# Kernel optimization log

Measured on AMD Instinct MI355X. Metric: run time of the kernel, lower is better.

## Reference

```python
import jax, jax.numpy as jnp
import numpy as np

NV, NSEG, SEGSZ, GRID = 778, 16, 49, 32
SCALE_FACTOR = 0.1


def grid_sample_3d(vol, pts):
    """Trilinear grid_sample, align_corners=True, zeros padding.
    vol: [D,H,W]; pts: [N,3] with (x,y,z) in [-1,1] (x indexes W, z indexes D).
    """
    D, H, W = vol.shape
    fx = (pts[:, 0] + 1.0) * 0.5 * (W - 1)
    fy = (pts[:, 1] + 1.0) * 0.5 * (H - 1)
    fz = (pts[:, 2] + 1.0) * 0.5 * (D - 1)
    x0f, y0f, z0f = jnp.floor(fx), jnp.floor(fy), jnp.floor(fz)
    wx, wy, wz = fx - x0f, fy - y0f, fz - z0f
    x0 = x0f.astype(jnp.int32)
    y0 = y0f.astype(jnp.int32)
    z0 = z0f.astype(jnp.int32)
    out = jnp.zeros(pts.shape[0], vol.dtype)
    for dz in (0, 1):
        zz = z0 + dz
        ww_z = wz if dz else (1.0 - wz)
        for dy in (0, 1):
            yy = y0 + dy
            ww_zy = ww_z * (wy if dy else (1.0 - wy))
            for dx in (0, 1):
                xx = x0 + dx
                w = ww_zy * (wx if dx else (1.0 - wx))
                valid = (xx >= 0) & (xx < W) & (yy >= 0) & (yy < H) & (zz >= 0) & (zz < D)
                v = vol[jnp.clip(zz, 0, D - 1), jnp.clip(yy, 0, H - 1), jnp.clip(xx, 0, W - 1)]
                out = out + jnp.where(valid, v, 0.0) * w
    return out


def _boxes(segv):
    # segv: [B,16,S,3] -> center [B,16,3], scale [B,16]  (no_grad in original)
    mn = segv.min(axis=2)
    mx = segv.max(axis=2)
    center = 0.5 * (mn + mx)                       # mean of (min, max)
    scale = (1.0 + SCALE_FACTOR) * 0.5 * (mx - mn).max(axis=-1)
    return jax.lax.stop_gradient(center), jax.lax.stop_gradient(scale)


def _cross_sample(seg_src, center, scale, phi, seg):
    # seg_src [B,I,S,3]; center [B,J,3]; scale [B,J]; phi [J,B,G,G,G]
    B = seg_src.shape[0]
    coords = (seg_src[:, :, None, :, :] - center[:, None, :, None, :]) / scale[:, None, :, None, None]
    pts = coords.transpose(2, 0, 1, 3, 4).reshape(NSEG, B, NSEG * SEGSZ, 3)  # [J,B,M,3]
    vals = jax.vmap(jax.vmap(grid_sample_3d))(phi, pts)                      # [J,B,M]
    vals = vals.reshape(NSEG, B, NSEG, SEGSZ).transpose(1, 2, 0, 3)          # [B,I,J,S]
    phisum = vals.sum(axis=2)                                                # [B,I,S]
    orisum = (vals * scale[:, None, :, None]).sum(axis=2)                    # [B,I,S]
    flat = seg.reshape(-1)
    out = jnp.zeros((B, NV), jnp.float32).at[:, flat].add(phisum.reshape(B, -1))
    ori = jnp.zeros((B, NV), jnp.float32).at[:, flat].add(orisum.reshape(B, -1))
    return out, ori


def setup_inputs() -> dict:
    key = jax.random.key(0)
    k1, k2, k3, k4 = jax.random.split(key, 4)
    bs = 128
    vertices = jax.random.normal(k1, (bs, 2, NV, 3), dtype=jnp.float32)
    seg = jax.random.randint(k2, (NSEG, SEGSZ), 0, NV).astype(jnp.int32)
    phi_right = jax.random.uniform(k3, (NSEG, bs, GRID, GRID, GRID), dtype=jnp.float32)
    phi_left = jax.random.uniform(k4, (NSEG, bs, GRID, GRID, GRID), dtype=jnp.float32)
    return {"vertices": vertices, "phi_right": phi_right, "phi_left": phi_left, "seg": seg}


def reference(vertices, phi_right, phi_left, seg):
    left_vert = vertices[:, 1]   # [B,778,3]
    right_vert = vertices[:, 0]
    segL = left_vert[:, seg]     # [B,16,S,3]
    segR = right_vert[:, seg]
    cL, sL = _boxes(segL)
    cR, sR = _boxes(segR)
    out_left, _ = _cross_sample(segL, cR, sR, phi_right, seg)
    out_right, _ = _cross_sample(segR, cL, sL, phi_left, seg)
    num_hand = 2
    loss = (out_left / num_hand ** 2 + out_right / num_hand ** 2).sum(axis=1)  # [B]
    return loss
```

## Files before the change

kernel.cpp:

```cpp
#include <hip/hip_runtime.h>

#define NVV   778
#define NSEG  16
#define SEGSZ 49
#define GRIDN 32
#define BATCH 128
#define NPTS  (NSEG * SEGSZ)
#define VOLSZ (GRIDN * GRIDN * GRIDN)
#define NBLK  256
#define VPB   16

#define HF (16 * 1024)

typedef __attribute__((address_space(1))) const void* as1_t;
typedef __attribute__((address_space(3))) void* as3_t;

#define STREAM(DST, SRC) \
    { _Pragma("unroll") \
      for (int c_ = 0; c_ < 4; ++c_) { \
        int ch_ = c_ * 16 + wv; \
        __builtin_amdgcn_global_load_lds( \
            (as1_t)((SRC) + ch_ * 256 + lane * 4), \
            (as3_t)((DST) + ch_ * 256), 16, 0, 0); \
      } }

__device__ __forceinline__ float tapxy(const float* slab, int x0, int y0,
                                       float wx, float wy)
{
    float s = 0.f;
    #pragma unroll
    for (int dy = 0; dy < 2; ++dy) {
        int yy = y0 + dy;
        if (yy < 0 || yy >= GRIDN) continue;
        float wyv = dy ? wy : 1.f - wy;
        const float* row = slab + yy * GRIDN;
        #pragma unroll
        for (int dx = 0; dx < 2; ++dx) {
            int xx = x0 + dx;
            if (xx < 0 || xx >= GRIDN) continue;
            s += wyv * (dx ? wx : 1.f - wx) * row[xx];
        }
    }
    return s;
}

__global__ __launch_bounds__(1024, 4) void sample_kernel(
    const float* __restrict__ vertices, const int* __restrict__ seg,
    const float* __restrict__ phiR, const float* __restrict__ phiL,
    float* __restrict__ loss)
{
    __shared__ __align__(16) float R0[HF];
    __shared__ __align__(16) float R1[HF];
    __shared__ float4 sbox[VPB];
    __shared__ float wsum[16];

    const int tid  = threadIdx.x;
    const int bx   = blockIdx.x;
    const int k    = bx & (NSEG - 1);
    const int wv   = tid >> 6;
    const int lane = tid & 63;

    auto phiPtr = [&](int it) {
        int vid  = bx + NBLK * it;
        int b    = (vid >> 4) & (BATCH - 1);
        int pass = vid >> 11;
        return (pass == 0 ? phiR : phiL) + ((size_t)k * BATCH + b) * VOLSZ;
    };

    int pvi = (tid < NPTS) ? seg[tid] : 0;

    int vidw    = bx + NBLK * wv;
    int bbw     = (vidw >> 4) & (BATCH - 1);
    int boxSide = ((vidw >> 11) == 0) ? 0 : 1;
    bool bact   = lane < SEGSZ;
    int bvi     = bact ? seg[k * SEGSZ + lane] : 0;
    const float* bvp = vertices + (((size_t)bbw * 2 + boxSide) * NVV + bvi) * 3;
    float bxx = bvp[0], bxy = bvp[1], bxz = bvp[2];

    float pvx = 0.f, pvy = 0.f, pvz = 0.f;
    if (tid < NPTS) {
        int b0 = (bx >> 4) & (BATCH - 1);
        const float* v = vertices + (((size_t)b0 * 2 + 1) * NVV + pvi) * 3;
        pvx = v[0]; pvy = v[1]; pvz = v[2];
    }

    STREAM(R0, phiPtr(0))

    {
        float mnx = bact ? bxx : 1e30f, mxx = bact ? bxx : -1e30f;
        float mny = bact ? bxy : 1e30f, mxy = bact ? bxy : -1e30f;
        float mnz = bact ? bxz : 1e30f, mxz = bact ? bxz : -1e30f;
        #pragma unroll
        for (int m = 32; m; m >>= 1) {
            mnx = fminf(mnx, __shfl_xor(mnx, m));
            mxx = fmaxf(mxx, __shfl_xor(mxx, m));
            mny = fminf(mny, __shfl_xor(mny, m));
            mxy = fmaxf(mxy, __shfl_xor(mxy, m));
            mnz = fminf(mnz, __shfl_xor(mnz, m));
            mxz = fmaxf(mxz, __shfl_xor(mxz, m));
        }
        if (lane == 0) {
            float ext = fmaxf(fmaxf(mxx - mnx, mxy - mny), mxz - mnz);
            sbox[wv] = make_float4(0.5f * (mnx + mxx), 0.5f * (mny + mxy),
                                   0.5f * (mnz + mxz), 1.0f / (0.55f * ext));
        }
    }

    __syncthreads();

    float nvx = 0.f, nvy = 0.f, nvz = 0.f;

    for (int v = 0; v < VPB; ++v) {
        const bool more = (v + 1 < VPB);

        if (v > 0 && tid == 0) {
            float tot = 0.f;
            #pragma unroll
            for (int i = 0; i < 16; ++i) tot += wsum[i];
            int vidp = bx + NBLK * (v - 1);
            atomicAdd(loss + ((vidp >> 4) & (BATCH - 1)), tot * 0.25f);
        }

        float fx = 0.f, fy = 0.f, fz = -2.f;
        if (tid < NPTS) {
            float4 b4 = sbox[v];
            fx = ((pvx - b4.x) * b4.w + 1.f) * 15.5f;
            fy = ((pvy - b4.y) * b4.w + 1.f) * 15.5f;
            fz = ((pvz - b4.z) * b4.w + 1.f) * 15.5f;
        }
        bool active = (fx > -1.f && fx < 32.f && fy > -1.f && fy < 32.f &&
                       fz > -1.f && fz < 32.f);
        float x0f = floorf(fx), y0f = floorf(fy), z0f = floorf(fz);
        float wx = fx - x0f, wy = fy - y0f, wz = fz - z0f;
        int x0 = (int)x0f, y0 = (int)y0f, z0 = (int)z0f;

        STREAM(R1, phiPtr(v) + HF)

        float acc = 0.f;
        if (active && z0 <= 15) {
            if (z0 >= 0)
                acc += (1.f - wz) * tapxy(R0 + z0 * 1024, x0, y0, wx, wy);
            if (z0 <= 14)
                acc += wz * tapxy(R0 + (z0 + 1) * 1024, x0, y0, wx, wy);
        }

        __syncthreads();

        if (more && tid < NPTS) {
            int vid  = bx + NBLK * (v + 1);
            int b_   = (vid >> 4) & (BATCH - 1);
            int srcS = (vid >> 11) == 0 ? 1 : 0;
            const float* vp = vertices + (((size_t)b_ * 2 + srcS) * NVV + pvi) * 3;
            nvx = vp[0]; nvy = vp[1]; nvz = vp[2];
        }
        if (more) { STREAM(R0, phiPtr(v + 1)) }

        if (active && z0 >= 15) {
            if (z0 >= 16)
                acc += (1.f - wz) * tapxy(R1 + (z0 - 16) * 1024, x0, y0, wx, wy);
            if (z0 <= 30)
                acc += wz * tapxy(R1 + (z0 - 15) * 1024, x0, y0, wx, wy);
        }

        #pragma unroll
        for (int off = 32; off; off >>= 1)
            acc += __shfl_down(acc, off);
        if (lane == 0) wsum[wv] = acc;

        __syncthreads();
        pvx = nvx; pvy = nvy; pvz = nvz;
    }

    if (tid == 0) {
        float tot = 0.f;
        #pragma unroll
        for (int i = 0; i < 16; ++i) tot += wsum[i];
        int vidp = bx + NBLK * (VPB - 1);
        atomicAdd(loss + ((vidp >> 4) & (BATCH - 1)), tot * 0.25f);
    }
}

extern "C" void kernel_launch(void* const* d_in, const int* in_sizes, int n_in,
                              void* d_out, int out_size, void* d_ws, size_t ws_size,
                              hipStream_t stream) {
    const float* vertices = (const float*)d_in[0];
    const float* phiR     = (const float*)d_in[1];
    const float* phiL     = (const float*)d_in[2];
    const int*   seg      = (const int*)d_in[3];
    float* loss = (float*)d_out;

    hipMemsetAsync(d_out, 0, (size_t)out_size * sizeof(float), stream);

    sample_kernel<<<NBLK, 1024, 0, stream>>>(vertices, seg, phiR, phiL, loss);
}
```

Before: 107.7 us.

## Split block into producer waves streaming phi and consumer waves sampling

```diff
diff --git a/kernel.cpp b/kernel.cpp
--- a/kernel.cpp
+++ b/kernel.cpp
@@ -17,8 +17,8 @@
 
 #define STREAM(DST, SRC) \
     { _Pragma("unroll") \
-      for (int c_ = 0; c_ < 4; ++c_) { \
-        int ch_ = c_ * 16 + wv; \
+      for (int c_ = 0; c_ < 8; ++c_) { \
+        int ch_ = c_ * 8 + wv; \
         __builtin_amdgcn_global_load_lds( \
             (as1_t)((SRC) + ch_ * 256 + lane * 4), \
             (as3_t)((DST) + ch_ * 256), 16, 0, 0); \
@@ -49,16 +49,18 @@
     const float* __restrict__ phiR, const float* __restrict__ phiL,
     float* __restrict__ loss)
 {
-    __shared__ __align__(16) float R0[HF];
-    __shared__ __align__(16) float R1[HF];
+    __shared__ __align__(16) float B0[HF];
+    __shared__ __align__(16) float B1[HF];
     __shared__ float4 sbox[VPB];
-    __shared__ float wsum[16];
+    __shared__ float wsum[8];
 
     const int tid  = threadIdx.x;
     const int bx   = blockIdx.x;
     const int k    = bx & (NSEG - 1);
     const int wv   = tid >> 6;
     const int lane = tid & 63;
+    const bool producer = (wv < 8);
+    const int ct   = tid - 512;
 
     auto phiPtr = [&](int it) {
         int vid  = bx + NBLK * it;
@@ -66,30 +68,32 @@
         int pass = vid >> 11;
         return (pass == 0 ? phiR : phiL) + ((size_t)k * BATCH + b) * VOLSZ;
     };
-
-    int pvi = (tid < NPTS) ? seg[tid] : 0;
-
-    int vidw    = bx + NBLK * wv;
-    int bbw     = (vidw >> 4) & (BATCH - 1);
-    int boxSide = ((vidw >> 11) == 0) ? 0 : 1;
-    bool bact   = lane < SEGSZ;
-    int bvi     = bact ? seg[k * SEGSZ + lane] : 0;
-    const float* bvp = vertices + (((size_t)bbw * 2 + boxSide) * NVV + bvi) * 3;
-    float bxx = bvp[0], bxy = bvp[1], bxz = bvp[2];
-
-    float pvx = 0.f, pvy = 0.f, pvz = 0.f;
-    if (tid < NPTS) {
-        int b0 = (bx >> 4) & (BATCH - 1);
-        const float* v = vertices + (((size_t)b0 * 2 + 1) * NVV + pvi) * 3;
-        pvx = v[0]; pvy = v[1]; pvz = v[2];
-    }
-
-    STREAM(R0, phiPtr(0))
+    auto vertBase = [&](int it) {
+        int vid  = bx + NBLK * it;
+        int b    = (vid >> 4) & (BATCH - 1);
+        int srcS = (vid >> 11) == 0 ? 1 : 0;
+        return vertices + ((size_t)b * 2 + srcS) * NVV * 3;
+    };
+
+    int pvi1 = 0, pvi2 = 0;
+    bool has2 = false;
+    if (!producer) {
+        pvi1 = seg[ct];
+        has2 = (ct + 512) < NPTS;
+        pvi2 = has2 ? seg[ct + 512] : 0;
+    }
 
     {
-        float mnx = bact ? bxx : 1e30f, mxx = bact ? bxx : -1e30f;
-        float mny = bact ? bxy : 1e30f, mxy = bact ? bxy : -1e30f;
-        float mnz = bact ? bxz : 1e30f, mxz = bact ? bxz : -1e30f;
+        int vidw    = bx + NBLK * wv;
+        int bbw     = (vidw >> 4) & (BATCH - 1);
+        int boxSide = ((vidw >> 11) == 0) ? 0 : 1;
+        bool bact   = lane < SEGSZ;
+        int bvi     = bact ? seg[k * SEGSZ + lane] : 0;
+        const float* bvp = vertices + (((size_t)bbw * 2 + boxSide) * NVV + bvi) * 3;
+        float x = bvp[0], y = bvp[1], z = bvp[2];
+        float mnx = bact ? x : 1e30f, mxx = bact ? x : -1e30f;
+        float mny = bact ? y : 1e30f, mxy = bact ? y : -1e30f;
+        float mnz = bact ? z : 1e30f, mxz = bact ? z : -1e30f;
         #pragma unroll
         for (int m = 32; m; m >>= 1) {
             mnx = fminf(mnx, __shfl_xor(mnx, m));
@@ -106,75 +110,113 @@
         }
     }
 
+    float p1x = 0.f, p1y = 0.f, p1z = 0.f;
+    float p2x = 0.f, p2y = 0.f, p2z = 0.f;
+    if (!producer) {
+        const float* vb = vertBase(0);
+        p1x = vb[pvi1 * 3 + 0]; p1y = vb[pvi1 * 3 + 1]; p1z = vb[pvi1 * 3 + 2];
+        if (has2) {
+            p2x = vb[pvi2 * 3 + 0]; p2y = vb[pvi2 * 3 + 1]; p2z = vb[pvi2 * 3 + 2];
+        }
+    }
+
+    if (producer) { STREAM(B0, phiPtr(0)) }
+
     __syncthreads();
 
-    float nvx = 0.f, nvy = 0.f, nvz = 0.f;
+    float n1x = 0.f, n1y = 0.f, n1z = 0.f;
+    float n2x = 0.f, n2y = 0.f, n2z = 0.f;
 
     for (int v = 0; v < VPB; ++v) {
         const bool more = (v + 1 < VPB);
 
-        if (v > 0 && tid == 0) {
-            float tot = 0.f;
+        float f1x = 0.f, f1y = 0.f, f1z = -2.f;
+        float f2x = 0.f, f2y = 0.f, f2z = -2.f;
+        if (!producer) {
+            float4 b4 = sbox[v];
+            f1x = ((p1x - b4.x) * b4.w + 1.f) * 15.5f;
+            f1y = ((p1y - b4.y) * b4.w + 1.f) * 15.5f;
+            f1z = ((p1z - b4.z) * b4.w + 1.f) * 15.5f;
+            if (has2) {
+                f2x = ((p2x - b4.x) * b4.w + 1.f) * 15.5f;
+                f2y = ((p2y - b4.y) * b4.w + 1.f) * 15.5f;
+                f2z = ((p2z - b4.z) * b4.w + 1.f) * 15.5f;
+            }
+        }
+        bool a1 = (f1x > -1.f && f1x < 32.f && f1y > -1.f && f1y < 32.f &&
+                   f1z > -1.f && f1z < 32.f);
+        bool a2 = (f2x > -1.f && f2x < 32.f && f2y > -1.f && f2y < 32.f &&
+                   f2z > -1.f && f2z < 32.f);
+        float x1f = floorf(f1x), y1f = floorf(f1y), z1f = floorf(f1z);
+        float x2f = floorf(f2x), y2f = floorf(f2y), z2f = floorf(f2z);
+        float w1x = f1x - x1f, w1y = f1y - y1f, w1z = f1z - z1f;
+        float w2x = f2x - x2f, w2y = f2y - y2f, w2z = f2z - z2f;
+        int x1 = (int)x1f, y1 = (int)y1f, z1 = (int)z1f;
+        int x2 = (int)x2f, y2 = (int)y2f, z2 = (int)z2f;
+        float acc1 = 0.f, acc2 = 0.f;
+
+        if (producer) {
+            STREAM(B1, phiPtr(v) + HF)
+        } else {
+            if (v > 0 && ct == 0) {
+                float tot = 0.f;
+                #pragma unroll
+                for (int i = 0; i < 8; ++i) tot += wsum[i];
+                int vidp = bx + NBLK * (v - 1);
+                atomicAdd(loss + ((vidp >> 4) & (BATCH - 1)), tot * 0.25f);
+            }
+            if (a1 && z1 <= 15) {
+                if (z1 >= 0)
+                    acc1 += (1.f - w1z) * tapxy(B0 + z1 * 1024, x1, y1, w1x, w1y);
+                if (z1 <= 14)
+                    acc1 += w1z * tapxy(B0 + (z1 + 1) * 1024, x1, y1, w1x, w1y);
+            }
+            if (a2 && z2 <= 15) {
+                if (z2 >= 0)
+                    acc2 += (1.f - w2z) * tapxy(B0 + z2 * 1024, x2, y2, w2x, w2y);
+                if (z2 <= 14)
+                    acc2 += w2z * tapxy(B0 + (z2 + 1) * 1024, x2, y2, w2x, w2y);
+            }
+            if (more) {
+                const float* vb = vertBase(v + 1);
+                n1x = vb[pvi1 * 3 + 0]; n1y = vb[pvi1 * 3 + 1]; n1z = vb[pvi1 * 3 + 2];
+                if (has2) {
+                    n2x = vb[pvi2 * 3 + 0]; n2y = vb[pvi2 * 3 + 1]; n2z = vb[pvi2 * 3 + 2];
+                }
+            }
+        }
+        __syncthreads();
+
+        if (producer) {
+            if (more) { STREAM(B0, phiPtr(v + 1)) }
+        } else {
+            if (a1 && z1 >= 15) {
+                if (z1 >= 16)
+                    acc1 += (1.f - w1z) * tapxy(B1 + (z1 - 16) * 1024, x1, y1, w1x, w1y);
+                if (z1 <= 30)
+                    acc1 += w1z * tapxy(B1 + (z1 - 15) * 1024, x1, y1, w1x, w1y);
+            }
+            if (a2 && z2 >= 15) {
+                if (z2 >= 16)
+                    acc2 += (1.f - w2z) * tapxy(B1 + (z2 - 16) * 1024, x2, y2, w2x, w2y);
+                if (z2 <= 30)
+                    acc2 += w2z * tapxy(B1 + (z2 - 15) * 1024, x2, y2, w2x, w2y);
+            }
+            float acc = acc1 + acc2;
             #pragma unroll
-            for (int i = 0; i < 16; ++i) tot += wsum[i];
-            int vidp = bx + NBLK * (v - 1);
-            atomicAdd(loss + ((vidp >> 4) & (BATCH - 1)), tot * 0.25f);
-        }
-
-        float fx = 0.f, fy = 0.f, fz = -2.f;
-        if (tid < NPTS) {
-            float4 b4 = sbox[v];
-            fx = ((pvx - b4.x) * b4.w + 1.f) * 15.5f;
-            fy = ((pvy - b4.y) * b4.w + 1.f) * 15.5f;
-            fz = ((pvz - b4.z) * b4.w + 1.f) * 15.5f;
-        }
-        bool active = (fx > -1.f && fx < 32.f && fy > -1.f && fy < 32.f &&
-                       fz > -1.f && fz < 32.f);
-        float x0f = floorf(fx), y0f = floorf(fy), z0f = floorf(fz);
-        float wx = fx - x0f, wy = fy - y0f, wz = fz - z0f;
-        int x0 = (int)x0f, y0 = (int)y0f, z0 = (int)z0f;
-
-        STREAM(R1, phiPtr(v) + HF)
-
-        float acc = 0.f;
-        if (active && z0 <= 15) {
-            if (z0 >= 0)
-                acc += (1.f - wz) * tapxy(R0 + z0 * 1024, x0, y0, wx, wy);
-            if (z0 <= 14)
-                acc += wz * tapxy(R0 + (z0 + 1) * 1024, x0, y0, wx, wy);
-        }
-
+            for (int off = 32; off; off >>= 1)
+                acc += __shfl_down(acc, off);
+            if (lane == 0) wsum[wv - 8] = acc;
+        }
         __syncthreads();
-
-        if (more && tid < NPTS) {
-            int vid  = bx + NBLK * (v + 1);
-            int b_   = (vid >> 4) & (BATCH - 1);
-            int srcS = (vid >> 11) == 0 ? 1 : 0;
-            const float* vp = vertices + (((size_t)b_ * 2 + srcS) * NVV + pvi) * 3;
-            nvx = vp[0]; nvy = vp[1]; nvz = vp[2];
-        }
-        if (more) { STREAM(R0, phiPtr(v + 1)) }
-
-        if (active && z0 >= 15) {
-            if (z0 >= 16)
-                acc += (1.f - wz) * tapxy(R1 + (z0 - 16) * 1024, x0, y0, wx, wy);
-            if (z0 <= 30)
-                acc += wz * tapxy(R1 + (z0 - 15) * 1024, x0, y0, wx, wy);
-        }
-
-        #pragma unroll
-        for (int off = 32; off; off >>= 1)
-            acc += __shfl_down(acc, off);
-        if (lane == 0) wsum[wv] = acc;
-
-        __syncthreads();
-        pvx = nvx; pvy = nvy; pvz = nvz;
-    }
-
-    if (tid == 0) {
+        p1x = n1x; p1y = n1y; p1z = n1z;
+        p2x = n2x; p2y = n2y; p2z = n2z;
+    }
+
+    if (!producer && ct == 0) {
         float tot = 0.f;
         #pragma unroll
-        for (int i = 0; i < 16; ++i) tot += wsum[i];
+        for (int i = 0; i < 8; ++i) tot += wsum[i];
         int vidp = bx + NBLK * (VPB - 1);
         atomicAdd(loss + ((vidp >> 4) & (BATCH - 1)), tot * 0.25f);
     }
```

After: 108.0 us. No clear change (+0.3%).
